# Optimization experiments

Measured on AMD Instinct MI355X. Metric: run time of the kernel, lower is better.

Reference implementation:

```python
import jax, jax.numpy as jnp
import numpy as np

K = 10  # knn neighbors
GF = 100  # gf_num = 25*4


def setup_inputs() -> dict:
    key = jax.random.key(0)
    ks = jax.random.split(key, 14)
    B, N = 4, 8192
    s = 0.1
    inp = {
        "x": jax.random.normal(ks[0], (B, N, 3), dtype=jnp.float32),
        # conv1: (3+K)->20->GF, 1x1 convs == per-point linears
        "w1a": jax.random.normal(ks[1], (3 + K, 20), jnp.float32) * s,
        "b1a": jax.random.normal(ks[2], (20,), jnp.float32) * s,
        "w1b": jax.random.normal(ks[3], (20, GF), jnp.float32) * s,
        "b1b": jax.random.normal(ks[4], (GF,), jnp.float32) * s,
        # conv2: GF->GF
        "w2": jax.random.normal(ks[5], (GF, GF), jnp.float32) * s,
        "b2": jax.random.normal(ks[6], (GF,), jnp.float32) * s,
        # conv3: 2*GF->20->10->2
        "w3a": jax.random.normal(ks[7], (2 * GF, 20), jnp.float32) * s,
        "b3a": jax.random.normal(ks[8], (20,), jnp.float32) * s,
        "w3b": jax.random.normal(ks[9], (20, 10), jnp.float32) * s,
        "b3b": jax.random.normal(ks[10], (10,), jnp.float32) * s,
        "w3c": jax.random.normal(ks[11], (10, 2), jnp.float32) * s,
        "b3c": jax.random.normal(ks[12], (2,), jnp.float32) * s,
    }
    return inp


def reference(x, w1a, b1a, w1b, b1b, w2, b2, w3a, b3a, w3b, b3b, w3c, b3c):
    # pairwise squared distances: [B, N, N]
    sq = jnp.sum(x * x, axis=-1)
    d = sq[:, :, None] + sq[:, None, :] - 2.0 * jnp.einsum("bnc,bmc->bnm", x, x)
    # k smallest distances per point, ascending order (matches torch topk largest=False)
    topk = -jax.lax.top_k(-d, K)[0]  # [B, N, K]
    h = jnp.concatenate([x, topk], axis=-1)  # [B, N, 3+K]
    # conv1 (1x1 convs == per-point linears)
    x1 = jax.nn.relu(jax.nn.relu(h @ w1a + b1a) @ w1b + b1b)  # [B, N, GF]
    # conv2
    x2 = jax.nn.relu(x1 @ w2 + b2)  # [B, N, GF]
    # global avg pool over points, broadcast back
    pool = jnp.mean(x2, axis=1, keepdims=True)  # [B, 1, GF]
    N = x1.shape[1]
    feat = jnp.concatenate([x1, jnp.broadcast_to(pool, (x1.shape[0], N, pool.shape[-1]))], axis=-1)
    # conv3 head + log-softmax over the 2 classes (torch dim=-2 on [B,2,N] layout)
    o = jax.nn.relu(feat @ w3a + b3a)
    o = jax.nn.relu(o @ w3b + b3b)
    o = o @ w3c + b3c  # [B, N, 2]
    return jax.nn.log_softmax(o, axis=-1)
```

## Files before the change

### kernel.cpp

```cpp
#include <hip/hip_runtime.h>
#include <math.h>

#define N_PTS   8192
#define NBATCH  4
#define NQ      (N_PTS*NBATCH)
#define GFN     100
#define KNN     10
#define NSPLIT  16
#define SPLITL  (N_PTS/NSPLIT)
#define QPL     4
#define MBLK    128
#define WROW    112

__device__ __forceinline__ float med3f(float a, float b, float c){
  return __builtin_amdgcn_fmed3f(a, b, c);
}

__device__ __forceinline__ void insert10(float (&m)[KNN], float d){
  #pragma unroll
  for (int k = KNN-1; k > 0; k--) m[k] = med3f(d, m[k-1], m[k]);
  m[0] = fminf(m[0], d);
}

__device__ __forceinline__ void ld7(float4 (&w)[7], const float* base){
  const float4* v = reinterpret_cast<const float4*>(base);
  #pragma unroll
  for (int i = 0; i < 7; i++) w[i] = v[i];
}

__device__ __forceinline__ void fma25(float (&acc)[25], float xv, const float4 (&w)[7]){
  #pragma unroll
  for (int i = 0; i < 6; i++){
    acc[i*4+0] = fmaf(xv, w[i].x, acc[i*4+0]);
    acc[i*4+1] = fmaf(xv, w[i].y, acc[i*4+1]);
    acc[i*4+2] = fmaf(xv, w[i].z, acc[i*4+2]);
    acc[i*4+3] = fmaf(xv, w[i].w, acc[i*4+3]);
  }
  acc[24] = fmaf(xv, w[6].x, acc[24]);
}

__global__ __launch_bounds__(256) void prep_kernel(const float* __restrict__ w1b,
                                                   const float* __restrict__ w2,
                                                   float* __restrict__ w1bp,
                                                   float* __restrict__ w2p,
                                                   float* __restrict__ pool){
  const int t0 = blockIdx.x * 256 + threadIdx.x;
  const int stride = gridDim.x * 256;
  for (int i = t0; i < 20*WROW; i += stride){
    int c = i / WROW, j = i % WROW, ch = j / 28, k = j % 28;
    w1bp[i] = (k < 25) ? w1b[c*GFN + ch*25 + k] : 0.0f;
  }
  for (int i = t0; i < GFN*WROW; i += stride){
    int c = i / WROW, j = i % WROW, ch = j / 28, k = j % 28;
    w2p[i] = (k < 25) ? w2[c*GFN + ch*25 + k] : 0.0f;
  }
  for (int i = t0; i < NBATCH*GFN; i += stride) pool[i] = 0.0f;
}

__global__ __launch_bounds__(256) void knn_kernel(const float* __restrict__ x,
                                                  float* __restrict__ cand){
  __shared__ float4 tile[SPLITL];
  const int t   = threadIdx.x;
  const int w   = t >> 6;
  const int p   = t & 63;
  const int s   = blockIdx.y;
  const int qb0 = blockIdx.x * 1024;
  const int b   = qb0 >> 13;
  const float* xb = x + (size_t)b * N_PTS * 3;

  #pragma unroll
  for (int k = 0; k < 2; k++){
    const int j = t + 256*k;
    const float* ps = xb + (size_t)(s*SPLITL + j)*3;
    float px = ps[0], py = ps[1], pz = ps[2];
    tile[j] = make_float4(px, py, pz, fmaf(pz, pz, fmaf(py, py, px*px)));
  }
  __syncthreads();

  float qx[QPL], qy[QPL], qz[QPL], qs[QPL];
  #pragma unroll
  for (int u = 0; u < QPL; u++){
    const int q = qb0 + w*256 + u*64 + p;
    qx[u] = x[(size_t)q*3+0];
    qy[u] = x[(size_t)q*3+1];
    qz[u] = x[(size_t)q*3+2];
    qs[u] = fmaf(qz[u], qz[u], fmaf(qy[u], qy[u], qx[u]*qx[u]));
  }

  float m[QPL][KNN];
  #pragma unroll
  for (int u = 0; u < QPL; u++)
    #pragma unroll
    for (int k = 0; k < KNN; k++) m[u][k] = INFINITY;

  #pragma unroll 4
  for (int j = 0; j < SPLITL; j++){
    float4 pt = tile[j];
    #pragma unroll
    for (int u = 0; u < QPL; u++){
      float dot = fmaf(qz[u], pt.z, fmaf(qy[u], pt.y, qx[u]*pt.x));
      float d   = fmaf(-2.0f, dot, qs[u] + pt.w);
      insert10(m[u], d);
    }
  }

  #pragma unroll
  for (int u = 0; u < QPL; u++){
    const int q = qb0 + w*256 + u*64 + p;
    #pragma unroll
    for (int k = 0; k < KNN; k++) cand[(size_t)(s*KNN + k)*NQ + q] = m[u][k];
  }
}

__global__ __launch_bounds__(512) void mlp1_kernel(
    const float* __restrict__ x,    const float* __restrict__ cand,
    const float* __restrict__ w1a,  const float* __restrict__ b1a,
    const float* __restrict__ w1bp, const float* __restrict__ b1b,
    const float* __restrict__ w2p,  const float* __restrict__ b2,
    float* __restrict__ x1r, float* __restrict__ pool){
  __shared__ float t20s[MBLK*21];
  __shared__ float x1s[MBLK*101];
  const int t = threadIdx.x;
  const int p = t & 63;
  const int g = __builtin_amdgcn_readfirstlane(t >> 6);
  const int half = g >> 2;
  const int sub  = g & 3;
  const int ph = half*64 + p;
  const int q0 = blockIdx.x * MBLK;
  const int q  = q0 + ph;
  const int b  = q0 >> 13;

  float* pa = x1s;
  {
    float m[KNN];
    #pragma unroll
    for (int k = 0; k < KNN; k++) m[k] = INFINITY;
    const int i0 = sub*40;
    #pragma unroll 8
    for (int i = i0; i < i0+40; i++) insert10(m, cand[(size_t)i*NQ + q]);
    #pragma unroll
    for (int k = 0; k < KNN; k++) pa[(g*64+p)*11 + k] = m[k];
  }
  __syncthreads();

  if (sub == 0){
    float mm[KNN];
    #pragma unroll
    for (int k = 0; k < KNN; k++) mm[k] = pa[(g*64+p)*11 + k];
    #pragma unroll
    for (int s2 = 1; s2 < 4; s2++)
      #pragma unroll
      for (int k = 0; k < KNN; k++)
        insert10(mm, pa[((half*4+s2)*64+p)*11 + k]);

    float h[13];
    h[0] = x[(size_t)q*3+0]; h[1] = x[(size_t)q*3+1]; h[2] = x[(size_t)q*3+2];
    #pragma unroll
    for (int k = 0; k < KNN; k++) h[3+k] = mm[k];

    float a[20];
    #pragma unroll
    for (int o = 0; o < 20; o++) a[o] = b1a[o];
    #pragma unroll
    for (int c = 0; c < 13; c++){
      float hv = h[c];
      #pragma unroll
      for (int o = 0; o < 20; o++) a[o] = fmaf(hv, w1a[c*20+o], a[o]);
    }
    #pragma unroll
    for (int o = 0; o < 20; o++) t20s[ph*21 + o] = fmaxf(a[o], 0.0f);
  }
  __syncthreads();

  const int o0 = sub * 25;
  float acc[25];

  #pragma unroll
  for (int k = 0; k < 25; k++) acc[k] = b1b[o0+k];
  #pragma unroll 2
  for (int c = 0; c < 20; c++){
    float tv = t20s[ph*21 + c];
    float4 wv[7];
    ld7(wv, w1bp + c*WROW + sub*28);
    fma25(acc, tv, wv);
  }
  #pragma unroll
  for (int k = 0; k < 25; k++){
    float v = fmaxf(acc[k], 0.0f);
    x1s[ph*101 + o0 + k] = v;
    x1r[(size_t)q*GFN + o0 + k] = v;
  }
  __syncthreads();

  #pragma unroll
  for (int k = 0; k < 25; k++) acc[k] = b2[o0+k];
  {
    float4 A[7], Bv[7];
    ld7(A, w2p + 0*WROW + sub*28);
    #pragma unroll 1
    for (int c = 0; c < GFN; c += 2){
      ld7(Bv, w2p + (c+1)*WROW + sub*28);
      float xv = x1s[ph*101 + c];
      fma25(acc, xv, A);
      if (c + 2 < GFN) ld7(A, w2p + (c+2)*WROW + sub*28);
      float xv2 = x1s[ph*101 + c + 1];
      fma25(acc, xv2, Bv);
    }
  }
  #pragma unroll
  for (int k = 0; k < 25; k++){
    float v = fmaxf(acc[k], 0.0f);
    #pragma unroll
    for (int off = 1; off < 64; off <<= 1) v += __shfl_xor(v, off);
    if (p == 0) atomicAdd(&pool[b*GFN + o0 + k], v);
  }
}

__global__ __launch_bounds__(128) void head_kernel(
    const float* __restrict__ x1r, const float* __restrict__ pool,
    const float* __restrict__ w3a, const float* __restrict__ b3a,
    const float* __restrict__ w3b, const float* __restrict__ b3b,
    const float* __restrict__ w3c, const float* __restrict__ b3c,
    float* __restrict__ out){
  __shared__ float poolm[GFN];
  __shared__ float poolpart[20];
  const int t = threadIdx.x;
  const int q = blockIdx.x * 128 + t;
  const int b = q >> 13;

  if (t < GFN) poolm[t] = pool[b*GFN+t] * (1.0f / (float)N_PTS);
  __syncthreads();
  if (t < 20){
    float a = b3a[t];
    for (int c = 0; c < GFN; c++) a = fmaf(poolm[c], w3a[(GFN+c)*20+t], a);
    poolpart[t] = a;
  }
  __syncthreads();

  float acc[20];
  #pragma unroll
  for (int o = 0; o < 20; o++) acc[o] = 0.0f;
  const float4* xr = reinterpret_cast<const float4*>(x1r + (size_t)q*GFN);
  #pragma unroll 5
  for (int c4 = 0; c4 < 25; c4++){
    float4 v = xr[c4];
    const float* wr = w3a + c4*4*20;
    #pragma unroll
    for (int o = 0; o < 20; o++) acc[o] = fmaf(v.x, wr[o],    acc[o]);
    #pragma unroll
    for (int o = 0; o < 20; o++) acc[o] = fmaf(v.y, wr[20+o], acc[o]);
    #pragma unroll
    for (int o = 0; o < 20; o++) acc[o] = fmaf(v.z, wr[40+o], acc[o]);
    #pragma unroll
    for (int o = 0; o < 20; o++) acc[o] = fmaf(v.w, wr[60+o], acc[o]);
  }
  float o1[20];
  #pragma unroll
  for (int o = 0; o < 20; o++) o1[o] = fmaxf(acc[o] + poolpart[o], 0.0f);

  float o2[10];
  #pragma unroll
  for (int o = 0; o < 10; o++){
    float a = b3b[o];
    #pragma unroll
    for (int c = 0; c < 20; c++) a = fmaf(o1[c], w3b[c*10+o], a);
    o2[o] = fmaxf(a, 0.0f);
  }
  float e0 = b3c[0], e1 = b3c[1];
  #pragma unroll
  for (int c = 0; c < 10; c++){
    e0 = fmaf(o2[c], w3c[c*2+0], e0);
    e1 = fmaf(o2[c], w3c[c*2+1], e1);
  }
  float mx = fmaxf(e0, e1);
  float a0 = e0 - mx, a1 = e1 - mx;
  float lse = logf(expf(a0) + expf(a1));
  float2 r; r.x = a0 - lse; r.y = a1 - lse;
  *reinterpret_cast<float2*>(out + (size_t)q*2) = r;
}

extern "C" void kernel_launch(void* const* d_in, const int* in_sizes, int n_in,
                              void* d_out, int out_size, void* d_ws, size_t ws_size,
                              hipStream_t stream) {
  const float* x   = (const float*)d_in[0];
  const float* w1a = (const float*)d_in[1];
  const float* b1a = (const float*)d_in[2];
  const float* w1b = (const float*)d_in[3];
  const float* b1b = (const float*)d_in[4];
  const float* w2  = (const float*)d_in[5];
  const float* b2  = (const float*)d_in[6];
  const float* w3a = (const float*)d_in[7];
  const float* b3a = (const float*)d_in[8];
  const float* w3b = (const float*)d_in[9];
  const float* b3b = (const float*)d_in[10];
  const float* w3c = (const float*)d_in[11];
  const float* b3c = (const float*)d_in[12];
  float* out = (float*)d_out;

  char* ws = (char*)d_ws;
  size_t off = 0;
  float* cand = (float*)(ws + off); off += (size_t)NQ*NSPLIT*KNN*4;
  float* x1r  = (float*)(ws + off); off += (size_t)NQ*GFN*4;
  float* pool = (float*)(ws + off); off += 4096;
  float* w1bp = (float*)(ws + off); off += (size_t)20*WROW*4;
  float* w2p  = (float*)(ws + off); off += (size_t)GFN*WROW*4;

  prep_kernel<<<16, 256, 0, stream>>>(w1b, w2, w1bp, w2p, pool);
  knn_kernel<<<dim3(NQ/1024, NSPLIT), 256, 0, stream>>>(x, cand);
  mlp1_kernel<<<NQ/MBLK, 512, 0, stream>>>(x, cand, w1a, b1a, w1bp, b1b, w2p, b2, x1r, pool);
  head_kernel<<<NQ/128, 128, 0, stream>>>(x1r, pool, w3a, b3a, w3b, b3b, w3c, b3c, out);
}
```

Before: 285.2 us.

## Halve queries per thread in KNN, redistribute MLP work, transpose x1 layout

The KNN kernel now handles two queries per thread instead of four, which doubles the grid so more waves can hide latency. The MLP kernel now uses 64 points per 256-thread block. Every wave finishes the top-k merge and runs the first linear layer redundantly in registers, which removes a shared-memory stage, a barrier and the idle waves of the old version. The x1 intermediate is now stored channel-major, so writes in the MLP kernel and reads in the head kernel are coalesced across threads. The cost is that the conv1a compute is repeated in every wave, and the KNN kernel does less reuse per tile load.

```diff
diff --git a/kernel.cpp b/kernel.cpp
--- a/kernel.cpp
+++ b/kernel.cpp
@@ -8,8 +8,8 @@
 #define KNN     10
 #define NSPLIT  16
 #define SPLITL  (N_PTS/NSPLIT)
-#define QPL     4
-#define MBLK    128
+#define QPL     2
+#define MBLK    64
 #define WROW    112
 
 __device__ __forceinline__ float med3f(float a, float b, float c){
@@ -64,7 +64,7 @@
   const int w   = t >> 6;
   const int p   = t & 63;
   const int s   = blockIdx.y;
-  const int qb0 = blockIdx.x * 1024;
+  const int qb0 = blockIdx.x * (256*QPL);
   const int b   = qb0 >> 13;
   const float* xb = x + (size_t)b * N_PTS * 3;
 
@@ -80,7 +80,7 @@
   float qx[QPL], qy[QPL], qz[QPL], qs[QPL];
   #pragma unroll
   for (int u = 0; u < QPL; u++){
-    const int q = qb0 + w*256 + u*64 + p;
+    const int q = qb0 + w*(64*QPL) + u*64 + p;
     qx[u] = x[(size_t)q*3+0];
     qy[u] = x[(size_t)q*3+1];
     qz[u] = x[(size_t)q*3+2];
@@ -106,89 +106,80 @@
 
   #pragma unroll
   for (int u = 0; u < QPL; u++){
-    const int q = qb0 + w*256 + u*64 + p;
+    const int q = qb0 + w*(64*QPL) + u*64 + p;
     #pragma unroll
     for (int k = 0; k < KNN; k++) cand[(size_t)(s*KNN + k)*NQ + q] = m[u][k];
   }
 }
 
-__global__ __launch_bounds__(512) void mlp1_kernel(
+__global__ __launch_bounds__(256) void mlp1_kernel(
     const float* __restrict__ x,    const float* __restrict__ cand,
     const float* __restrict__ w1a,  const float* __restrict__ b1a,
     const float* __restrict__ w1bp, const float* __restrict__ b1b,
     const float* __restrict__ w2p,  const float* __restrict__ b2,
-    float* __restrict__ x1r, float* __restrict__ pool){
-  __shared__ float t20s[MBLK*21];
+    float* __restrict__ x1t, float* __restrict__ pool){
+  __shared__ float pa[4*MBLK*11];
   __shared__ float x1s[MBLK*101];
   const int t = threadIdx.x;
   const int p = t & 63;
   const int g = __builtin_amdgcn_readfirstlane(t >> 6);
-  const int half = g >> 2;
-  const int sub  = g & 3;
-  const int ph = half*64 + p;
   const int q0 = blockIdx.x * MBLK;
-  const int q  = q0 + ph;
+  const int q  = q0 + p;
   const int b  = q0 >> 13;
 
-  float* pa = x1s;
+  float m[KNN];
+  #pragma unroll
+  for (int k = 0; k < KNN; k++) m[k] = INFINITY;
   {
-    float m[KNN];
-    #pragma unroll
-    for (int k = 0; k < KNN; k++) m[k] = INFINITY;
-    const int i0 = sub*40;
+    const int i0 = g*40;
     #pragma unroll 8
     for (int i = i0; i < i0+40; i++) insert10(m, cand[(size_t)i*NQ + q]);
     #pragma unroll
-    for (int k = 0; k < KNN; k++) pa[(g*64+p)*11 + k] = m[k];
-  }
-  __syncthreads();
-
-  if (sub == 0){
-    float mm[KNN];
-    #pragma unroll
-    for (int k = 0; k < KNN; k++) mm[k] = pa[(g*64+p)*11 + k];
-    #pragma unroll
-    for (int s2 = 1; s2 < 4; s2++)
+    for (int k = 0; k < KNN; k++) pa[(g*MBLK+p)*11 + k] = m[k];
+  }
+  __syncthreads();
+
+  #pragma unroll
+  for (int s2 = 0; s2 < 4; s2++){
+    if (s2 != g){
       #pragma unroll
-      for (int k = 0; k < KNN; k++)
-        insert10(mm, pa[((half*4+s2)*64+p)*11 + k]);
-
-    float h[13];
-    h[0] = x[(size_t)q*3+0]; h[1] = x[(size_t)q*3+1]; h[2] = x[(size_t)q*3+2];
-    #pragma unroll
-    for (int k = 0; k < KNN; k++) h[3+k] = mm[k];
-
-    float a[20];
-    #pragma unroll
-    for (int o = 0; o < 20; o++) a[o] = b1a[o];
-    #pragma unroll
-    for (int c = 0; c < 13; c++){
-      float hv = h[c];
-      #pragma unroll
-      for (int o = 0; o < 20; o++) a[o] = fmaf(hv, w1a[c*20+o], a[o]);
+      for (int k = 0; k < KNN; k++) insert10(m, pa[(s2*MBLK+p)*11 + k]);
     }
-    #pragma unroll
-    for (int o = 0; o < 20; o++) t20s[ph*21 + o] = fmaxf(a[o], 0.0f);
-  }
-  __syncthreads();
-
-  const int o0 = sub * 25;
+  }
+
+  float h[13];
+  h[0] = x[(size_t)q*3+0]; h[1] = x[(size_t)q*3+1]; h[2] = x[(size_t)q*3+2];
+  #pragma unroll
+  for (int k = 0; k < KNN; k++) h[3+k] = m[k];
+
+  float t20[20];
+  #pragma unroll
+  for (int o = 0; o < 20; o++) t20[o] = b1a[o];
+  #pragma unroll
+  for (int c = 0; c < 13; c++){
+    float hv = h[c];
+    #pragma unroll
+    for (int o = 0; o < 20; o++) t20[o] = fmaf(hv, w1a[c*20+o], t20[o]);
+  }
+  #pragma unroll
+  for (int o = 0; o < 20; o++) t20[o] = fmaxf(t20[o], 0.0f);
+
+  const int o0 = g * 25;
   float acc[25];
 
   #pragma unroll
   for (int k = 0; k < 25; k++) acc[k] = b1b[o0+k];
   #pragma unroll 2
   for (int c = 0; c < 20; c++){
-    float tv = t20s[ph*21 + c];
     float4 wv[7];
-    ld7(wv, w1bp + c*WROW + sub*28);
-    fma25(acc, tv, wv);
+    ld7(wv, w1bp + c*WROW + g*28);
+    fma25(acc, t20[c], wv);
   }
   #pragma unroll
   for (int k = 0; k < 25; k++){
     float v = fmaxf(acc[k], 0.0f);
-    x1s[ph*101 + o0 + k] = v;
-    x1r[(size_t)q*GFN + o0 + k] = v;
+    x1s[p*101 + o0 + k] = v;
+    x1t[(size_t)(o0+k)*NQ + q] = v;
   }
   __syncthreads();
 
@@ -196,14 +187,14 @@
   for (int k = 0; k < 25; k++) acc[k] = b2[o0+k];
   {
     float4 A[7], Bv[7];
-    ld7(A, w2p + 0*WROW + sub*28);
+    ld7(A, w2p + 0*WROW + g*28);
     #pragma unroll 1
     for (int c = 0; c < GFN; c += 2){
-      ld7(Bv, w2p + (c+1)*WROW + sub*28);
-      float xv = x1s[ph*101 + c];
+      ld7(Bv, w2p + (c+1)*WROW + g*28);
+      float xv = x1s[p*101 + c];
       fma25(acc, xv, A);
-      if (c + 2 < GFN) ld7(A, w2p + (c+2)*WROW + sub*28);
-      float xv2 = x1s[ph*101 + c + 1];
+      if (c + 2 < GFN) ld7(A, w2p + (c+2)*WROW + g*28);
+      float xv2 = x1s[p*101 + c + 1];
       fma25(acc, xv2, Bv);
     }
   }
@@ -217,7 +208,7 @@
 }
 
 __global__ __launch_bounds__(128) void head_kernel(
-    const float* __restrict__ x1r, const float* __restrict__ pool,
+    const float* __restrict__ x1t, const float* __restrict__ pool,
     const float* __restrict__ w3a, const float* __restrict__ b3a,
     const float* __restrict__ w3b, const float* __restrict__ b3b,
     const float* __restrict__ w3c, const float* __restrict__ b3c,
@@ -240,19 +231,11 @@
   float acc[20];
   #pragma unroll
   for (int o = 0; o < 20; o++) acc[o] = 0.0f;
-  const float4* xr = reinterpret_cast<const float4*>(x1r + (size_t)q*GFN);
-  #pragma unroll 5
-  for (int c4 = 0; c4 < 25; c4++){
-    float4 v = xr[c4];
-    const float* wr = w3a + c4*4*20;
-    #pragma unroll
-    for (int o = 0; o < 20; o++) acc[o] = fmaf(v.x, wr[o],    acc[o]);
-    #pragma unroll
-    for (int o = 0; o < 20; o++) acc[o] = fmaf(v.y, wr[20+o], acc[o]);
-    #pragma unroll
-    for (int o = 0; o < 20; o++) acc[o] = fmaf(v.z, wr[40+o], acc[o]);
-    #pragma unroll
-    for (int o = 0; o < 20; o++) acc[o] = fmaf(v.w, wr[60+o], acc[o]);
+  #pragma unroll 8
+  for (int c = 0; c < GFN; c++){
+    float xv = x1t[(size_t)c*NQ + q];
+    #pragma unroll
+    for (int o = 0; o < 20; o++) acc[o] = fmaf(xv, w3a[c*20+o], acc[o]);
   }
   float o1[20];
   #pragma unroll
@@ -300,13 +283,13 @@
   char* ws = (char*)d_ws;
   size_t off = 0;
   float* cand = (float*)(ws + off); off += (size_t)NQ*NSPLIT*KNN*4;
-  float* x1r  = (float*)(ws + off); off += (size_t)NQ*GFN*4;
+  float* x1t  = (float*)(ws + off); off += (size_t)NQ*GFN*4;
   float* pool = (float*)(ws + off); off += 4096;
   float* w1bp = (float*)(ws + off); off += (size_t)20*WROW*4;
   float* w2p  = (float*)(ws + off); off += (size_t)GFN*WROW*4;
 
   prep_kernel<<<16, 256, 0, stream>>>(w1b, w2, w1bp, w2p, pool);
-  knn_kernel<<<dim3(NQ/1024, NSPLIT), 256, 0, stream>>>(x, cand);
-  mlp1_kernel<<<NQ/MBLK, 512, 0, stream>>>(x, cand, w1a, b1a, w1bp, b1b, w2p, b2, x1r, pool);
-  head_kernel<<<NQ/128, 128, 0, stream>>>(x1r, pool, w3a, b3a, w3b, b3b, w3c, b3c, out);
-}
+  knn_kernel<<<dim3(NQ/(256*QPL), NSPLIT), 256, 0, stream>>>(x, cand);
+  mlp1_kernel<<<NQ/MBLK, 256, 0, stream>>>(x, cand, w1a, b1a, w1bp, b1b, w2p, b2, x1t, pool);
+  head_kernel<<<NQ/128, 128, 0, stream>>>(x1t, pool, w3a, b3a, w3b, b3b, w3c, b3c, out);
+}
```

New measurement: 285.3 us. Within noise of the previous version (+0.0%).
